# Optimization experiments

Hardware: AMD Instinct MI355X
Metric: run time of the kernel (lower is better)

## Reference

```python
import jax, jax.numpy as jnp
import numpy as np

T, B, P, E, H = 64, 32, 32, 128, 128


def setup_inputs() -> dict:
    key = jax.random.key(0)
    ks = jax.random.split(key, 32)
    def rn(i, shape, s=1.0):
        return jax.random.normal(ks[i], shape, dtype=jnp.float32) * s
    w = 0.08  # small init scale for params
    return {
        "ped_obs_traj": rn(0, (T, B, 2, P)),
        "ped_obs_traj_rel": rn(1, (T, B, 2, P)),
        "ped_vx": rn(2, (T, B, 1, P)),
        "ped_vy": rn(3, (T, B, 1, P)),
        "ped_ax": rn(4, (T, B, 1, P)),
        "ped_ay": rn(5, (T, B, 1, P)),
        "ped_mask": jax.random.randint(ks[6], (T, B, 1, P), 0, 2, dtype=jnp.int32),
        # spatial / state embeddings (torch Linear: weight (out,in))
        "W_sp": rn(7, (E, 2), w), "b_sp": rn(8, (E,), w),
        "W_st": rn(9, (E, 4), w), "b_st": rn(10, (E,), w),
        # trajectory LSTM (gate order i,f,g,o)
        "Wih_t": rn(11, (4 * H, E), w), "Whh_t": rn(12, (4 * H, H), w),
        "bih_t": rn(13, (4 * H,), w), "bhh_t": rn(14, (4 * H,), w),
        # state LSTM
        "Wih_s": rn(15, (4 * H, E), w), "Whh_s": rn(16, (4 * H, H), w),
        "bih_s": rn(17, (4 * H,), w), "bhh_s": rn(18, (4 * H,), w),
        # attention MLP: Linear(2H,H)+ReLU, Linear(H,1)+ReLU
        "A1": rn(19, (H, 2 * H), w), "a1": rn(20, (H,), w),
        "A2": rn(21, (1, H), w), "a2": rn(22, (1,), w),
        # fusion MLP: Linear(2H,H)+ReLU, Linear(H,H)+ReLU
        "F1": rn(23, (H, 2 * H), w), "f1": rn(24, (H,), w),
        "F2": rn(25, (H, H), w), "f2": rn(26, (H,), w),
    }


def _masked_lstm(x_emb, mask, Wih, Whh, bih, bhh):
    """LSTM over time, holding (h,c) where mask==False. Equivalent to running
    the LSTM on the compacted valid subsequence from a zero initial state.
    x_emb: (T,N,E), mask: (T,N) bool -> final h: (N,H)."""
    N = x_emb.shape[1]
    Hd = Whh.shape[1]
    # precompute input projection for all steps (T,N,4H)
    xp = jnp.einsum('tne,ge->tng', x_emb, Wih) + bih + bhh
    def step(carry, inp):
        h, c = carry
        g, m = inp
        gates = g + h @ Whh.T
        i, f, gg, o = jnp.split(gates, 4, axis=-1)
        c_new = jax.nn.sigmoid(f) * c + jax.nn.sigmoid(i) * jnp.tanh(gg)
        h_new = jax.nn.sigmoid(o) * jnp.tanh(c_new)
        m = m[:, None]
        return (jnp.where(m, h_new, h), jnp.where(m, c_new, c)), None
    init = (jnp.zeros((N, Hd), x_emb.dtype), jnp.zeros((N, Hd), x_emb.dtype))
    (h, _), _ = jax.lax.scan(step, init, (xp, mask))
    return h


def reference(ped_obs_traj, ped_obs_traj_rel, ped_vx, ped_vy, ped_ax, ped_ay, ped_mask,
              W_sp, b_sp, W_st, b_st,
              Wih_t, Whh_t, bih_t, bhh_t,
              Wih_s, Whh_s, bih_s, bhh_s,
              A1, a1, A2, a2, F1, f1, F2, f2):
    T_, B_, _, P_ = ped_obs_traj_rel.shape
    N = B_ * P_
    Hd = Whh_t.shape[1]
    # flatten (batch, pedestrian) into one ragged batch axis N
    traj = jnp.transpose(ped_obs_traj_rel, (0, 1, 3, 2)).reshape(T_, N, 2)
    state = jnp.transpose(
        jnp.concatenate([ped_vx, ped_vy, ped_ax, ped_ay], axis=2), (0, 1, 3, 2)
    ).reshape(T_, N, 4)
    mask = jnp.transpose(ped_mask, (0, 1, 3, 2)).reshape(T_, N) > 0

    emb_t = traj @ W_sp.T + b_sp      # (T,N,E)
    emb_s = state @ W_st.T + b_st     # (T,N,E)
    h_t = _masked_lstm(emb_t, mask, Wih_t, Whh_t, bih_t, bhh_t)  # (N,H)
    h_s = _masked_lstm(emb_s, mask, Wih_s, Whh_s, bih_s, bhh_s)  # (N,H)

    # pedestrian participates only if it has >= 2 valid timesteps
    ok = mask.sum(0) >= 2  # (N,)
    comb = jnp.concatenate([h_t, h_s], axis=1)  # (N,2H)
    fused = jax.nn.relu(jax.nn.relu(comb @ F1.T + f1) @ F2.T + f2)  # (N,H)
    fused = jnp.where(ok[:, None], fused, 0.0).reshape(B_, P_, Hd)
    okb = ok.reshape(B_, P_)

    nv = okb.sum(1, keepdims=True).astype(fused.dtype)  # (B,1) valid count
    mean = fused.sum(1) / jnp.maximum(nv, 1.0)           # (B,H) mean over valid
    att_in = jnp.concatenate(
        [fused, jnp.broadcast_to(mean[:, None, :], fused.shape)], axis=2)  # (B,P,2H)
    scores = jax.nn.relu(
        jax.nn.relu(att_in @ A1.T + a1) @ A2.T + a2)[..., 0]  # (B,P)
    # masked softmax over valid pedestrians (n==1 -> weight 1; n==0 -> all 0)
    s = jnp.where(okb, scores, -1e9)
    e = jnp.where(okb, jnp.exp(s - s.max(1, keepdims=True)), 0.0)
    w = e / jnp.maximum(e.sum(1, keepdims=True), 1e-9)
    enc = jnp.einsum('bp,bph->bh', w, fused)  # (B,H)
    return enc[None]  # (num_layers=1, B, H)
```

## Files before the change

### kernel.cpp

```cpp
#include <hip/hip_runtime.h>

#define T_ 64
#define B_ 32
#define P_ 32
#define N_ 1024
#define H_ 128
#define G_ 512

typedef __attribute__((ext_vector_type(8))) _Float16 half8;
typedef __attribute__((ext_vector_type(4))) float f32x4;

__device__ __forceinline__ float rcpf(float x){ return __builtin_amdgcn_rcpf(x); }
__device__ __forceinline__ float sigm(float x){ return rcpf(1.f+__expf(-x)); }
__device__ __forceinline__ float tanh_fast(float x){ return 1.f - 2.f*rcpf(__expf(2.f*x)+1.f); }

__global__ __launch_bounds__(256) void prep_kernel(
    const float* __restrict__ W_sp, const float* __restrict__ b_sp,
    const float* __restrict__ W_st, const float* __restrict__ b_st,
    const float* __restrict__ Wih_t, const float* __restrict__ Whh_t,
    const float* __restrict__ bih_t, const float* __restrict__ bhh_t,
    const float* __restrict__ Wih_s, const float* __restrict__ Whh_s,
    const float* __restrict__ bih_s, const float* __restrict__ bhh_s,
    const float* __restrict__ F1, const float* __restrict__ F2,
    const float* __restrict__ A1,
    _Float16* __restrict__ Wfrag, _Float16* __restrict__ Bxfrag,
    _Float16* __restrict__ F1frag, _Float16* __restrict__ F2frag,
    _Float16* __restrict__ A1frag)
{
  __shared__ float Wl[128][129];
  __shared__ float spw[512];
  __shared__ float bsm[128];
  __shared__ float prt[128][8];

  const int tid = threadIdx.x;
  const int blk = blockIdx.x;

  if (blk < 8) {
    const int L = blk >> 2, q = blk & 3;
    const int g0 = q*128;
    const float* Wih = L ? Wih_s : Wih_t;
    {
      unsigned int* Bz = (unsigned int*)Bxfrag;
      for (int i = tid; i < 2048; i += 256){
        const int wv = i >> 8, word = i & 255;
        Bz[((L*8+wv)*4+q)*256 + word] = 0u;
      }
    }
    if (L == 0){
      if (tid < 256) spw[tid] = W_sp[tid];
      if (tid < 128) bsm[tid] = b_sp[tid];
    } else {
      spw[tid] = W_st[tid]; spw[256+tid] = W_st[256+tid];
      if (tid < 128) bsm[tid] = b_st[tid];
    }
    for (int idx = tid; idx < 4096; idx += 256){
      const int r = idx >> 5, c4 = idx & 31;
      const float4 v = *(const float4*)(Wih + (size_t)(g0+r)*H_ + c4*4);
      Wl[r][c4*4+0]=v.x; Wl[r][c4*4+1]=v.y; Wl[r][c4*4+2]=v.z; Wl[r][c4*4+3]=v.w;
    }
    __syncthreads();
    const int g_l = tid & 127, half = tid >> 7, e0 = half*64;
    float a0=0.f,a1v=0.f,a2=0.f,a3=0.f,ab=0.f;
    if (L == 0){
      for (int e=e0; e<e0+64; ++e){
        const float wv = Wl[g_l][e];
        a0 += wv*spw[e*2]; a1v += wv*spw[e*2+1]; ab += wv*bsm[e];
      }
    } else {
      for (int e=e0; e<e0+64; ++e){
        const float wv = Wl[g_l][e];
        a0 += wv*spw[e*4]; a1v += wv*spw[e*4+1]; a2 += wv*spw[e*4+2]; a3 += wv*spw[e*4+3];
        ab += wv*bsm[e];
      }
    }
    if (half == 1){ prt[g_l][0]=a0; prt[g_l][1]=a1v; prt[g_l][2]=a2; prt[g_l][3]=a3; prt[g_l][4]=ab; }
    __syncthreads();
    if (half == 0){
      a0 += prt[g_l][0]; a1v += prt[g_l][1]; a2 += prt[g_l][2]; a3 += prt[g_l][3]; ab += prt[g_l][4];
      const int g = g0 + g_l;
      const float bsum = ab + (L ? bih_s[g] : bih_t[g]) + (L ? bhh_s[g] : bhh_t[g]);
      const int wv = g_l >> 4, lane = g_l & 15;
      _Float16* dst = Bxfrag + (size_t)(((L*8+wv)*4+q)*64 + lane)*8;
      if (L == 0){
        dst[0]=(_Float16)a0; dst[1]=(_Float16)a1v; dst[2]=(_Float16)0.f; dst[3]=(_Float16)0.f;
      } else {
        dst[0]=(_Float16)a0; dst[1]=(_Float16)a1v; dst[2]=(_Float16)a2; dst[3]=(_Float16)a3;
      }
      const _Float16 bh = (_Float16)bsum;
      dst[4]=bh; dst[5]=(_Float16)(bsum-(float)bh);
    }
  } else if (blk < 72) {
    const int tb = blk - 8;
    const int L  = tb >> 5;
    const float* Whh = L ? Whh_s : Whh_t;
    const int g0 = (tb & 3)*128 + ((tb>>2)&7)*16;
    #pragma unroll
    for (int i=0;i<8;i++){
      const int fidx = tid + i*256;
      const int r = fidx >> 7, c = fidx & 127;
      Wl[r][c] = Whh[(size_t)(g0+r)*H_ + c];
    }
    __syncthreads();
    const int l = tid & 63, t = tid >> 6;
    const int rr = l & 15, kb = t*32 + 8*(l>>4);
    half8 v;
    #pragma unroll
    for (int j=0;j<8;j++) v[j] = (_Float16)Wl[rr][kb+j];
    *(half8*)(Wfrag + (size_t)((tb*4 + t)*64 + l)*8) = v;
  } else {
    const int fb = blk - 72;
    const int btype = fb >> 3;
    const int nt = fb & 7;
    const float* src = (btype==0) ? F1 : (btype==1) ? F2 : A1;
    _Float16* dstf   = (btype==0) ? F1frag : (btype==1) ? F2frag : A1frag;
    const int K = (btype==1) ? 128 : 256;
    float* S = &Wl[0][0];
    const int nf4 = 16*K/4;
    for (int i = tid; i < nf4; i += 256){
      const int r = i / (K/4), c4 = i % (K/4);
      const float4 v = *(const float4*)(src + (size_t)(nt*16+r)*K + c4*4);
      S[r*257 + c4*4+0]=v.x; S[r*257 + c4*4+1]=v.y;
      S[r*257 + c4*4+2]=v.z; S[r*257 + c4*4+3]=v.w;
    }
    __syncthreads();
    const int nkt = K/32;
    for (int s = tid; s < nkt*64; s += 256){
      const int kt = s >> 6, l = s & 63;
      half8 v;
      #pragma unroll
      for (int jj=0;jj<8;jj++)
        v[jj] = (_Float16)S[(l&15)*257 + kt*32 + 8*(l>>4) + jj];
      *(half8*)(dstf + (size_t)((nt*nkt + kt)*64 + l)*8) = v;
    }
  }
}

__global__ __launch_bounds__(512) __attribute__((amdgpu_waves_per_eu(2,2)))
void lstm_kernel(
    const float* __restrict__ rel, const float* __restrict__ pvx,
    const float* __restrict__ pvy, const float* __restrict__ pax,
    const float* __restrict__ pay, const int* __restrict__ maskI,
    const _Float16* __restrict__ Wfrag, const _Float16* __restrict__ Bxfrag,
    float* __restrict__ h_t_out, float* __restrict__ h_s_out)
{
  __shared__ _Float16 hA[2][4][64][8] __align__(16);
  __shared__ _Float16 axf[T_][16][8] __align__(16);
  __shared__ _Float16 zslot[8] __align__(16);
  __shared__ unsigned int ml[T_];

  const int lstm = blockIdx.y;
  const int tid  = threadIdx.x;
  const int w    = tid >> 6;
  const int l    = tid & 63;
  const int n0   = blockIdx.x * 8;
  const int u    = w*16 + (l & 15);
  const int kt_u = u >> 5;

  half8 bw[4][4], bx[4];
  #pragma unroll
  for (int n=0;n<4;n++){
    #pragma unroll
    for (int t=0;t<4;t++){
      const int base = ((((lstm*8 + w)*4 + n)*4 + t)*64 + l)*8;
      bw[n][t] = *(const half8*)(Wfrag + base);
    }
    bx[n] = *(const half8*)(Bxfrag + (((lstm*8 + w)*4 + n)*64 + l)*8);
  }

  {
    const int t = tid >> 3, r = tid & 7;
    const int n = n0 + r, b = n >> 5, p = n & 31;
    float x0,x1,x2,x3;
    if (lstm == 0){
      x0 = rel[(t*B_+b)*64 + p]; x1 = rel[(t*B_+b)*64 + 32 + p];
      x2 = 0.f; x3 = 0.f;
    } else {
      const int i0 = t*N_ + n;
      x0 = pvx[i0]; x1 = pvy[i0]; x2 = pax[i0]; x3 = pay[i0];
    }
    half8 v;
    v[0]=(_Float16)x0; v[1]=(_Float16)x1; v[2]=(_Float16)x2; v[3]=(_Float16)x3;
    v[4]=(_Float16)1.f; v[5]=(_Float16)1.f; v[6]=(_Float16)0.f; v[7]=(_Float16)0.f;
    *(half8*)&axf[t][r][0] = v;
    half8 zz;
    #pragma unroll
    for (int q=0;q<8;q++) zz[q]=(_Float16)0.f;
    *(half8*)&axf[t][8+r][0] = zz;
    if (tid == 0) *(half8*)&zslot[0] = zz;
    if (tid < T_){
      unsigned int mw = 0;
      for (int rr=0; rr<8; rr++) mw |= (maskI[tid*N_ + n0 + rr] > 0) ? (1u<<rr) : 0u;
      ml[tid] = mw;
    }
  }
  {
    unsigned int* hz = (unsigned int*)&hA[0][0][0][0];
    #pragma unroll
    for (int i=0;i<4;i++) hz[tid + i*512] = 0u;
  }

  const int halfw = l >> 5;
  const int rbase = ((l & 31) >> 4)*4 + 2*halfw;
  const int lpp0  = rbase + 16*((u >> 3) & 3);
  const int hoff0 = kt_u*512 + lpp0*8 + (u & 7);
  const int hoff1 = hoff0 + 8;
  _Float16* hbase = &hA[0][0][0][0];
  const _Float16* axp_base = (l < 16) ? &axf[0][l][0] : &zslot[0];
  const int ax_stride = (l < 16) ? 128 : 0;

  float cc0 = 0.f, cc1 = 0.f;
  _Float16 rh0 = (_Float16)0.f, rh1 = (_Float16)0.f;
  __syncthreads();

  const f32x4 zc = {0.f, 0.f, 0.f, 0.f};
  #pragma unroll 2
  for (int t=0; t<T_; ++t){
    const int cur = t & 1, nxt = cur ^ 1;
    const unsigned int mw = ml[t];

    const half8 ax = *(const half8*)(axp_base + t*ax_stride);
    f32x4 acc[4];
    #pragma unroll
    for (int n=0;n<4;n++)
      acc[n] = __builtin_amdgcn_mfma_f32_16x16x32_f16(ax, bx[n], zc, 0, 0, 0);

    half8 ah[4];
    #pragma unroll
    for (int kt=0;kt<4;kt++) ah[kt] = *(const half8*)&hA[cur][kt][l][0];

    #pragma unroll
    for (int kt=0;kt<4;kt++)
      #pragma unroll
      for (int n=0;n<4;n++)
        acc[n] = __builtin_amdgcn_mfma_f32_16x16x32_f16(ah[kt], bw[n][kt], acc[n], 0, 0, 0);

    float g0[4], g1[4];
    #pragma unroll
    for (int n=0;n<4;n++){
      const float s2 = __shfl_xor(acc[n][2], 32, 64);
      const float s3 = __shfl_xor(acc[n][3], 32, 64);
      g0[n] = halfw ? s2 : acc[n][0];
      g1[n] = halfw ? s3 : acc[n][1];
    }

    {
      const float cn = sigm(g0[1])*cc0 + sigm(g0[0])*tanh_fast(g0[2]);
      const float hn = sigm(g0[3])*tanh_fast(cn);
      const int mb = (mw >> rbase) & 1;
      cc0 = mb ? cn : cc0;
      rh0 = mb ? (_Float16)hn : rh0;
      hbase[nxt*2048 + hoff0] = rh0;
    }
    {
      const float cn = sigm(g1[1])*cc1 + sigm(g1[0])*tanh_fast(g1[2]);
      const float hn = sigm(g1[3])*tanh_fast(cn);
      const int mb = (mw >> (rbase+1)) & 1;
      cc1 = mb ? cn : cc1;
      rh1 = mb ? (_Float16)hn : rh1;
      hbase[nxt*2048 + hoff1] = rh1;
    }
    __syncthreads();
  }

  float* hout = lstm ? h_s_out : h_t_out;
  hout[(n0 + rbase    )*H_ + u] = (float)rh0;
  hout[(n0 + rbase + 1)*H_ + u] = (float)rh1;
}

__global__ __launch_bounds__(512) void head_kernel(
    const float* __restrict__ h_t, const float* __restrict__ h_s,
    const int* __restrict__ maskI,
    const _Float16* __restrict__ F1frag, const float* __restrict__ f1,
    const _Float16* __restrict__ F2frag, const float* __restrict__ f2,
    const _Float16* __restrict__ A1frag, const float* __restrict__ a1,
    const float* __restrict__ A2, const float* __restrict__ a2v,
    float* __restrict__ out)
{
  extern __shared__ char hsm[];
  _Float16* combf = (_Float16*)hsm;
  _Float16* fusf  = (_Float16*)hsm;
  _Float16* hidf  = (_Float16*)(hsm + 32768);
  float* fus      = (float*)(hsm + 49152);
  float* meansh   = (float*)(hsm + 65664);
  float* okcnt    = (float*)(hsm + 66176);
  float* okv      = (float*)(hsm + 68224);
  float* sred     = (float*)(hsm + 68352);
  float* wgt      = (float*)(hsm + 68864);
  float* part     = (float*)(hsm + 68992);
  float* nvp      = (float*)(hsm + 71040);

  const int b = blockIdx.x, tid = threadIdx.x;
  const int w = tid >> 6, l = tid & 63;
  const int m = w >> 2;
  const int n0 = (w & 3) * 2;
  const int ccol = l & 15;

  #pragma unroll
  for (int it = 0; it < 4; ++it){
    const int slot = tid + it*512;
    const int r = slot >> 6, c4 = slot & 63;
    const float4 v = (c4 < 32)
      ? *(const float4*)(h_t + (size_t)(b*P_+r)*H_ + c4*4)
      : *(const float4*)(h_s + (size_t)(b*P_+r)*H_ + (c4-32)*4);
    const int mm = r >> 4, rl = r & 15;
    float vv[4] = {v.x, v.y, v.z, v.w};
    #pragma unroll
    for (int e=0;e<4;e++){
      const int k = c4*4 + e;
      const int lane = rl + 16*((k>>3)&3);
      const int jj = k & 7, kt = k >> 5;
      const _Float16 hi = (_Float16)vv[e];
      const _Float16 lo = (_Float16)(vv[e] - (float)hi);
      combf[(size_t)((mm*2+0)*8+kt)*512 + lane*8 + jj] = hi;
      combf[(size_t)((mm*2+1)*8+kt)*512 + lane*8 + jj] = lo;
    }
  }
  {
    const int p = tid >> 4, tt = tid & 15;
    int c = 0;
    #pragma unroll
    for (int q2=0;q2<4;q2++) c += (maskI[(tt*4+q2)*N_ + b*P_ + p] > 0);
    okcnt[p*16+tt] = (float)c;
  }
  __syncthreads();

  if (tid < 32){
    float c = 0.f;
    #pragma unroll
    for (int q2=0;q2<16;q2++) c += okcnt[tid*16+q2];
    const float ok = (c >= 2.f) ? 1.f : 0.f;
    okv[tid] = ok;
    float nvv = ok;
    #pragma unroll
    for (int off=16; off>=1; off>>=1) nvv += __shfl_xor(nvv, off, 32);
    if (tid == 0) nvp[0] = fmaxf(nvv, 1.f);
  }

  const f32x4 zc = {0.f,0.f,0.f,0.f};

  half8 ah[8], al[8];
  #pragma unroll
  for (int kt=0;kt<8;kt++){
    ah[kt] = *(const half8*)(combf + (size_t)((m*2+0)*8+kt)*512 + l*8);
    al[kt] = *(const half8*)(combf + (size_t)((m*2+1)*8+kt)*512 + l*8);
  }
  float hval[2][4];
  #pragma unroll
  for (int t2=0;t2<2;t2++){
    const int nt = n0 + t2;
    f32x4 acc = zc;
    #pragma unroll
    for (int kt=0;kt<8;kt++){
      const half8 bb = *(const half8*)(F1frag + (size_t)((nt*8+kt)*64 + l)*8);
      acc = __builtin_amdgcn_mfma_f32_16x16x32_f16(ah[kt], bb, acc, 0, 0, 0);
      acc = __builtin_amdgcn_mfma_f32_16x16x32_f16(al[kt], bb, acc, 0, 0, 0);
    }
    const float bias = f1[nt*16 + ccol];
    #pragma unroll
    for (int reg=0;reg<4;reg++) hval[t2][reg] = fmaxf(acc[reg] + bias, 0.f);
  }
  #pragma unroll
  for (int t2=0;t2<2;t2++){
    const int jb = (n0+t2)*16 + ccol;
    const int kt2 = jb >> 5, lgrp = 16*((jb>>3)&3), jj2 = jb & 7;
    #pragma unroll
    for (int reg=0;reg<4;reg++){
      const int row = (l>>4)*4 + reg;
      const float hv2 = hval[t2][reg];
      const _Float16 hi = (_Float16)hv2;
      hidf[(size_t)((m*2+0)*4+kt2)*512 + (row+lgrp)*8 + jj2] = hi;
      hidf[(size_t)((m*2+1)*4+kt2)*512 + (row+lgrp)*8 + jj2] = (_Float16)(hv2 - (float)hi);
    }
  }
  __syncthreads();

  half8 ah2[4], al2[4];
  #pragma unroll
  for (int kt=0;kt<4;kt++){
    ah2[kt] = *(const half8*)(hidf + (size_t)((m*2+0)*4+kt)*512 + l*8);
    al2[kt] = *(const half8*)(hidf + (size_t)((m*2+1)*4+kt)*512 + l*8);
  }
  #pragma unroll
  for (int t2=0;t2<2;t2++){
    const int nt = n0 + t2;
    f32x4 acc = zc;
    #pragma unroll
    for (int kt=0;kt<4;kt++){
      const half8 bb = *(const half8*)(F2frag + (size_t)((nt*4+kt)*64 + l)*8);
      acc = __builtin_amdgcn_mfma_f32_16x16x32_f16(ah2[kt], bb, acc, 0, 0, 0);
      acc = __builtin_amdgcn_mfma_f32_16x16x32_f16(al2[kt], bb, acc, 0, 0, 0);
    }
    const int j = nt*16 + ccol;
    const float bias = f2[j];
    const int kt2 = j >> 5, lgrp = 16*((j>>3)&3), jj2 = j & 7;
    #pragma unroll
    for (int reg=0;reg<4;reg++){
      const int row = (l>>4)*4 + reg;
      const int rowg = m*16 + row;
      const float fv = fmaxf(acc[reg] + bias, 0.f) * okv[rowg];
      fus[rowg*129 + j] = fv;
      const _Float16 hi = (_Float16)fv;
      fusf[(size_t)((m*2+0)*4+kt2)*512 + (row+lgrp)*8 + jj2] = hi;
      fusf[(size_t)((m*2+1)*4+kt2)*512 + (row+lgrp)*8 + jj2] = (_Float16)(fv - (float)hi);
    }
  }
  __syncthreads();

  if (tid < H_){
    float s = 0.f;
    #pragma unroll 8
    for (int r=0;r<P_;r++) s += fus[r*129 + tid];
    meansh[tid] = s * rcpf(nvp[0]);
  }
  __syncthreads();

  half8 af[4], alf[4], amh[4], aml[4];
  #pragma unroll
  for (int kt=0;kt<4;kt++){
    af[kt]  = *(const half8*)(fusf + (size_t)((m*2+0)*4+kt)*512 + l*8);
    alf[kt] = *(const half8*)(fusf + (size_t)((m*2+1)*4+kt)*512 + l*8);
    #pragma unroll
    for (int jj=0;jj<8;jj++){
      const float mv = meansh[kt*32 + 8*(l>>4) + jj];
      const _Float16 hi = (_Float16)mv;
      amh[kt][jj] = hi;
      aml[kt][jj] = (_Float16)(mv - (float)hi);
    }
  }
  float vsum[4] = {0.f,0.f,0.f,0.f};
  #pragma unroll
  for (int t2=0;t2<2;t2++){
    const int nt = n0 + t2;
    f32x4 acc = zc;
    #pragma unroll
    for (int kt=0;kt<4;kt++){
      const half8 bb = *(const half8*)(A1frag + (size_t)((nt*8+kt)*64 + l)*8);
      acc = __builtin_amdgcn_mfma_f32_16x16x32_f16(af[kt],  bb, acc, 0, 0, 0);
      acc = __builtin_amdgcn_mfma_f32_16x16x32_f16(alf[kt], bb, acc, 0, 0, 0);
    }
    #pragma unroll
    for (int kt=0;kt<4;kt++){
      const half8 bb = *(const half8*)(A1frag + (size_t)((nt*8+4+kt)*64 + l)*8);
      acc = __builtin_amdgcn_mfma_f32_16x16x32_f16(amh[kt], bb, acc, 0, 0, 0);
      acc = __builtin_amdgcn_mfma_f32_16x16x32_f16(aml[kt], bb, acc, 0, 0, 0);
    }
    const int j = nt*16 + ccol;
    const float b1 = a1[j], b2 = A2[j];
    #pragma unroll
    for (int reg=0;reg<4;reg++) vsum[reg] += fmaxf(acc[reg] + b1, 0.f) * b2;
  }
  #pragma unroll
  for (int off=1; off<16; off<<=1){
    #pragma unroll
    for (int reg=0;reg<4;reg++) vsum[reg] += __shfl_xor(vsum[reg], off, 64);
  }
  if (ccol == 0){
    #pragma unroll
    for (int reg=0;reg<4;reg++)
      sred[(m*16 + (l>>4)*4 + reg)*4 + (w&3)] = vsum[reg];
  }
  __syncthreads();

  if (tid < P_){
    float s = sred[tid*4+0]+sred[tid*4+1]+sred[tid*4+2]+sred[tid*4+3] + a2v[0];
    s = fmaxf(s, 0.f);
    s = (okv[tid] > 0.f) ? s : -1e9f;
    float mx = s;
    #pragma unroll
    for (int off=16; off>=1; off>>=1) mx = fmaxf(mx, __shfl_xor(mx, off, 32));
    const float e = (okv[tid] > 0.f) ? __expf(s - mx) : 0.f;
    float se = e;
    #pragma unroll
    for (int off=16; off>=1; off>>=1) se += __shfl_xor(se, off, 32);
    wgt[tid] = e * rcpf(fmaxf(se, 1e-9f));
  }
  __syncthreads();

  {
    const int rs = tid >> 7, j = tid & 127;
    float s = 0.f;
    #pragma unroll
    for (int r=rs*8; r<rs*8+8; ++r) s += wgt[r]*fus[r*129 + j];
    part[rs*128 + j] = s;
  }
  __syncthreads();
  if (tid < H_) out[b*H_ + tid] = part[0*128+tid]+part[1*128+tid]+part[2*128+tid]+part[3*128+tid];
}

extern "C" void kernel_launch(void* const* d_in, const int* in_sizes, int n_in,
                              void* d_out, int out_size, void* d_ws, size_t ws_size,
                              hipStream_t stream) {
  const float* rel   = (const float*)d_in[1];
  const float* pvx   = (const float*)d_in[2];
  const float* pvy   = (const float*)d_in[3];
  const float* pax   = (const float*)d_in[4];
  const float* pay   = (const float*)d_in[5];
  const int*   pmask = (const int*)  d_in[6];
  const float* W_sp  = (const float*)d_in[7];
  const float* b_sp  = (const float*)d_in[8];
  const float* W_st  = (const float*)d_in[9];
  const float* b_st  = (const float*)d_in[10];
  const float* Wih_t = (const float*)d_in[11];
  const float* Whh_t = (const float*)d_in[12];
  const float* bih_t = (const float*)d_in[13];
  const float* bhh_t = (const float*)d_in[14];
  const float* Wih_s = (const float*)d_in[15];
  const float* Whh_s = (const float*)d_in[16];
  const float* bih_s = (const float*)d_in[17];
  const float* bhh_s = (const float*)d_in[18];
  const float* A1    = (const float*)d_in[19];
  const float* a1    = (const float*)d_in[20];
  const float* A2    = (const float*)d_in[21];
  const float* a2v   = (const float*)d_in[22];
  const float* F1    = (const float*)d_in[23];
  const float* f1    = (const float*)d_in[24];
  const float* F2    = (const float*)d_in[25];
  const float* f2    = (const float*)d_in[26];

  float* ws = (float*)d_ws;
  size_t off = 0;
  _Float16* Wfrag  = (_Float16*)(ws + off); off += 65536;
  _Float16* Bxfrag = (_Float16*)(ws + off); off += 16384;
  _Float16* F1frag = (_Float16*)(ws + off); off += 16384;
  _Float16* F2frag = (_Float16*)(ws + off); off += 8192;
  _Float16* A1frag = (_Float16*)(ws + off); off += 16384;
  float* h_t    = ws + off; off += (size_t)N_*H_;
  float* h_s    = ws + off; off += (size_t)N_*H_;

  hipLaunchKernelGGL(prep_kernel, dim3(96), dim3(256), 0, stream,
      W_sp, b_sp, W_st, b_st, Wih_t, Whh_t, bih_t, bhh_t,
      Wih_s, Whh_s, bih_s, bhh_s, F1, F2, A1,
      Wfrag, Bxfrag, F1frag, F2frag, A1frag);

  hipLaunchKernelGGL(lstm_kernel, dim3(N_/8, 2), dim3(512), 0, stream,
      rel, pvx, pvy, pax, pay, pmask,
      Wfrag, Bxfrag, h_t, h_s);

  const int head_lds = 71680;
  hipFuncSetAttribute((const void*)head_kernel,
                      hipFuncAttributeMaxDynamicSharedMemorySize, head_lds);
  hipLaunchKernelGGL(head_kernel, dim3(B_), dim3(512), head_lds, stream,
      h_t, h_s, pmask, F1frag, f1, F2frag, f2, A1frag, a1, A2, a2v,
      (float*)d_out);
}
```

Measured before the change: 67.91 us.

## Split LSTM gate MFMA work across 16 waves with LDS gate exchange

```diff
diff --git a/kernel.cpp b/kernel.cpp
--- a/kernel.cpp
+++ b/kernel.cpp
@@ -135,7 +135,7 @@
   }
 }
 
-__global__ __launch_bounds__(512) __attribute__((amdgpu_waves_per_eu(2,2)))
+__global__ __launch_bounds__(1024) __attribute__((amdgpu_waves_per_eu(4,4)))
 void lstm_kernel(
     const float* __restrict__ rel, const float* __restrict__ pvx,
     const float* __restrict__ pvy, const float* __restrict__ pax,
@@ -146,28 +146,28 @@
   __shared__ _Float16 hA[2][4][64][8] __align__(16);
   __shared__ _Float16 axf[T_][16][8] __align__(16);
   __shared__ _Float16 zslot[8] __align__(16);
+  __shared__ float gbuf[8][516];
   __shared__ unsigned int ml[T_];
 
   const int lstm = blockIdx.y;
   const int tid  = threadIdx.x;
-  const int w    = tid >> 6;
+  const int wv   = tid >> 6;
   const int l    = tid & 63;
   const int n0   = blockIdx.x * 8;
-  const int u    = w*16 + (l & 15);
-  const int kt_u = u >> 5;
-
-  half8 bw[4][4], bx[4];
-  #pragma unroll
-  for (int n=0;n<4;n++){
-    #pragma unroll
-    for (int t=0;t<4;t++){
-      const int base = ((((lstm*8 + w)*4 + n)*4 + t)*64 + l)*8;
-      bw[n][t] = *(const half8*)(Wfrag + base);
-    }
-    bx[n] = *(const half8*)(Bxfrag + (((lstm*8 + w)*4 + n)*64 + l)*8);
-  }
-
-  {
+
+  half8 bw[2][4], bx[2];
+  #pragma unroll
+  for (int s=0;s<2;s++){
+    const int nf = 2*wv + s;
+    const int w8 = nf & 7, n4 = nf >> 3;
+    const int tb = lstm*32 + w8*4 + n4;
+    #pragma unroll
+    for (int t=0;t<4;t++)
+      bw[s][t] = *(const half8*)(Wfrag + (size_t)((tb*4 + t)*64 + l)*8);
+    bx[s] = *(const half8*)(Bxfrag + (size_t)(((lstm*8 + w8)*4 + n4)*64 + l)*8);
+  }
+
+  if (tid < 512){
     const int t = tid >> 3, r = tid & 7;
     const int n = n0 + r, b = n >> 5, p = n & 31;
     float x0,x1,x2,x3;
@@ -187,84 +187,76 @@
     for (int q=0;q<8;q++) zz[q]=(_Float16)0.f;
     *(half8*)&axf[t][8+r][0] = zz;
     if (tid == 0) *(half8*)&zslot[0] = zz;
-    if (tid < T_){
-      unsigned int mw = 0;
-      for (int rr=0; rr<8; rr++) mw |= (maskI[tid*N_ + n0 + rr] > 0) ? (1u<<rr) : 0u;
-      ml[tid] = mw;
-    }
+  }
+  if (tid < T_){
+    unsigned int mw = 0;
+    #pragma unroll
+    for (int rr=0; rr<8; rr++) mw |= (maskI[tid*N_ + n0 + rr] > 0) ? (1u<<rr) : 0u;
+    ml[tid] = mw;
   }
   {
     unsigned int* hz = (unsigned int*)&hA[0][0][0][0];
-    #pragma unroll
-    for (int i=0;i<4;i++) hz[tid + i*512] = 0u;
-  }
-
-  const int halfw = l >> 5;
-  const int rbase = ((l & 31) >> 4)*4 + 2*halfw;
-  const int lpp0  = rbase + 16*((u >> 3) & 3);
-  const int hoff0 = kt_u*512 + lpp0*8 + (u & 7);
-  const int hoff1 = hoff0 + 8;
+    hz[tid] = 0u;
+    if (tid < 1024) hz[tid + 1024] = 0u;
+  }
+
+  const int ar = tid & 7;
+  const int au = tid >> 3;
+  const int hoff = (au>>5)*512 + (ar + 16*((au>>3)&3))*8 + (au&7);
   _Float16* hbase = &hA[0][0][0][0];
   const _Float16* axp_base = (l < 16) ? &axf[0][l][0] : &zslot[0];
   const int ax_stride = (l < 16) ? 128 : 0;
-
-  float cc0 = 0.f, cc1 = 0.f;
-  _Float16 rh0 = (_Float16)0.f, rh1 = (_Float16)0.f;
+  const int col = l & 15, r0 = (l >> 4) * 4;
+
+  float cc = 0.f;
+  _Float16 rh = (_Float16)0.f;
   __syncthreads();
 
   const f32x4 zc = {0.f, 0.f, 0.f, 0.f};
-  #pragma unroll 2
   for (int t=0; t<T_; ++t){
     const int cur = t & 1, nxt = cur ^ 1;
+
+    const half8 ax = *(const half8*)(axp_base + t*ax_stride);
+    half8 ah[4];
+    #pragma unroll
+    for (int kt=0;kt<4;kt++) ah[kt] = *(const half8*)&hA[cur][kt][l][0];
+
+    f32x4 acc[2];
+    #pragma unroll
+    for (int s=0;s<2;s++){
+      acc[s] = __builtin_amdgcn_mfma_f32_16x16x32_f16(ax, bx[s], zc, 0, 0, 0);
+      #pragma unroll
+      for (int kt=0;kt<4;kt++)
+        acc[s] = __builtin_amdgcn_mfma_f32_16x16x32_f16(ah[kt], bw[s][kt], acc[s], 0, 0, 0);
+    }
+
+    if (l < 32){
+      #pragma unroll
+      for (int s=0;s<2;s++){
+        const int gg = (2*wv+s)*16 + col;
+        #pragma unroll
+        for (int reg=0;reg<4;reg++)
+          gbuf[r0+reg][gg] = acc[s][reg];
+      }
+    }
+    __syncthreads();
+
     const unsigned int mw = ml[t];
-
-    const half8 ax = *(const half8*)(axp_base + t*ax_stride);
-    f32x4 acc[4];
-    #pragma unroll
-    for (int n=0;n<4;n++)
-      acc[n] = __builtin_amdgcn_mfma_f32_16x16x32_f16(ax, bx[n], zc, 0, 0, 0);
-
-    half8 ah[4];
-    #pragma unroll
-    for (int kt=0;kt<4;kt++) ah[kt] = *(const half8*)&hA[cur][kt][l][0];
-
-    #pragma unroll
-    for (int kt=0;kt<4;kt++)
-      #pragma unroll
-      for (int n=0;n<4;n++)
-        acc[n] = __builtin_amdgcn_mfma_f32_16x16x32_f16(ah[kt], bw[n][kt], acc[n], 0, 0, 0);
-
-    float g0[4], g1[4];
-    #pragma unroll
-    for (int n=0;n<4;n++){
-      const float s2 = __shfl_xor(acc[n][2], 32, 64);
-      const float s3 = __shfl_xor(acc[n][3], 32, 64);
-      g0[n] = halfw ? s2 : acc[n][0];
-      g1[n] = halfw ? s3 : acc[n][1];
-    }
-
-    {
-      const float cn = sigm(g0[1])*cc0 + sigm(g0[0])*tanh_fast(g0[2]);
-      const float hn = sigm(g0[3])*tanh_fast(cn);
-      const int mb = (mw >> rbase) & 1;
-      cc0 = mb ? cn : cc0;
-      rh0 = mb ? (_Float16)hn : rh0;
-      hbase[nxt*2048 + hoff0] = rh0;
-    }
-    {
-      const float cn = sigm(g1[1])*cc1 + sigm(g1[0])*tanh_fast(g1[2]);
-      const float hn = sigm(g1[3])*tanh_fast(cn);
-      const int mb = (mw >> (rbase+1)) & 1;
-      cc1 = mb ? cn : cc1;
-      rh1 = mb ? (_Float16)hn : rh1;
-      hbase[nxt*2048 + hoff1] = rh1;
-    }
+    const float gi = gbuf[ar][0*128+au];
+    const float gf = gbuf[ar][1*128+au];
+    const float gv = gbuf[ar][2*128+au];
+    const float go = gbuf[ar][3*128+au];
+    const float cn = sigm(gf)*cc + sigm(gi)*tanh_fast(gv);
+    const float hn = sigm(go)*tanh_fast(cn);
+    const int mb = (mw >> ar) & 1;
+    cc = mb ? cn : cc;
+    rh = mb ? (_Float16)hn : rh;
+    hbase[nxt*2048 + hoff] = rh;
     __syncthreads();
   }
 
   float* hout = lstm ? h_s_out : h_t_out;
-  hout[(n0 + rbase    )*H_ + u] = (float)rh0;
-  hout[(n0 + rbase + 1)*H_ + u] = (float)rh1;
+  hout[(n0 + ar)*H_ + au] = (float)rh;
 }
 
 __global__ __launch_bounds__(512) void head_kernel(
@@ -532,7 +524,7 @@
       Wih_s, Whh_s, bih_s, bhh_s, F1, F2, A1,
       Wfrag, Bxfrag, F1frag, F2frag, A1frag);
 
-  hipLaunchKernelGGL(lstm_kernel, dim3(N_/8, 2), dim3(512), 0, stream,
+  hipLaunchKernelGGL(lstm_kernel, dim3(N_/8, 2), dim3(1024), 0, stream,
       rel, pvx, pvy, pax, pay, pmask,
       Wfrag, Bxfrag, h_t, h_s);
 
```

Result: slower. 78.45 us (+15.5%).
